# Performance work log

Measured on AMD Instinct MI355X. Metric: run time of the kernel, lower is better.

## Reference

```python
import jax, jax.numpy as jnp
import numpy as np

R = 8
EPS = 1e-08
EPSS = 1e-12


def _diff_x(x, r):
    left = x[:, :, r:2 * r + 1]
    middle = x[:, :, 2 * r + 1:] - x[:, :, :-2 * r - 1]
    right = x[:, :, -1:] - x[:, :, -2 * r - 1:-r - 1]
    return jnp.concatenate([left, middle, right], axis=2)


def _diff_y(x, r):
    left = x[:, :, :, r:2 * r + 1]
    middle = x[:, :, :, 2 * r + 1:] - x[:, :, :, :-2 * r - 1]
    right = x[:, :, :, -1:] - x[:, :, :, -2 * r - 1:-r - 1]
    return jnp.concatenate([left, middle, right], axis=3)


def box_filter(x, r):
    # cumsum-based (2r+1)x(2r+1) box sum with clamped borders (matches torch BoxFilter)
    return _diff_y(jnp.cumsum(_diff_x(jnp.cumsum(x, axis=2), r), axis=3), r)


def bilinear_resize(x, H, W):
    # F.interpolate(mode='bilinear', align_corners=True) for NCHW
    n, c, h, w = x.shape
    ys = jnp.linspace(0.0, h - 1.0, H)
    xs = jnp.linspace(0.0, w - 1.0, W)
    y0 = jnp.floor(ys).astype(jnp.int32)
    x0 = jnp.floor(xs).astype(jnp.int32)
    y1 = jnp.minimum(y0 + 1, h - 1)
    x1 = jnp.minimum(x0 + 1, w - 1)
    wy = (ys - y0).astype(x.dtype)[None, None, :, None]
    wx = (xs - x0).astype(x.dtype)[None, None, None, :]
    rows = jnp.take(x, y0, axis=2) * (1.0 - wy) + jnp.take(x, y1, axis=2) * wy
    return jnp.take(rows, x0, axis=3) * (1.0 - wx) + jnp.take(rows, x1, axis=3) * wx


def setup_inputs() -> dict:
    key = jax.random.key(0)
    k1, k2, k3, k4 = jax.random.split(key, 4)
    return {
        "lr_x": jax.random.normal(k1, (4, 3, 256, 256), dtype=jnp.float32),
        "lr_y": jax.random.normal(k2, (4, 3, 256, 256), dtype=jnp.float32),
        "hr_x": jax.random.normal(k3, (4, 3, 1024, 1024), dtype=jnp.float32),
        "l_a": jax.random.uniform(k4, (4, 3, 256, 256), dtype=jnp.float32),
    }


def reference(lr_x, lr_y, hr_x, l_a):
    n, c, h, w = lr_x.shape
    _, _, hh, wh = hr_x.shape
    dt = lr_x.dtype

    N = box_filter(jnp.ones((1, 1, h, w), dtype=dt), R)  # local window counts

    l_a = jnp.abs(l_a) + EPSS
    l_t = l_a / jnp.sum(l_a)

    mean_a = box_filter(l_a) if False else box_filter(l_a, R) / N
    mean_a2xy = box_filter(l_a * l_a * lr_x * lr_y, R) / N
    mean_tax = box_filter(l_t * l_a * lr_x, R) / N
    mean_ay = box_filter(l_a * lr_y, R) / N
    mean_a2x2 = box_filter(l_a * l_a * lr_x * lr_x, R) / N
    mean_ax = box_filter(l_a * lr_x, R) / N

    temp = jnp.abs(mean_a2x2 - N * mean_tax * mean_ax)
    A = (mean_a2xy - N * mean_tax * mean_ay) / (temp + EPS)
    b = (mean_ay - A * mean_ax) / mean_a

    A = box_filter(A, R) / N
    b = box_filter(b, R) / N

    mean_A = bilinear_resize(A, hh, wh)
    mean_b = bilinear_resize(b, hh, wh)
    return (mean_A * hr_x + mean_b).astype(jnp.float32)
```

## Files before the change

kernel.cpp:

```cpp
#include <hip/hip_runtime.h>

#define RAD 8
#define HH 256
#define WW 256
#define NC 12
#define PS (HH*WW)

__global__ __launch_bounds__(256) void k_hbox6(const float* __restrict__ la,
                                               const float* __restrict__ lx,
                                               const float* __restrict__ ly,
                                               float* __restrict__ Hbuf,
                                               float* __restrict__ sumS) {
    int p  = blockIdx.x >> 6;
    int rc = blockIdx.x & 63;
    int base = p * PS + rc * 4 * WW;
    int tid = threadIdx.x, lane = tid & 63, wid = tid >> 6;
    __shared__ float wtot[6][4];
    __shared__ float Pref[6][WW];
    __shared__ float ls[4];
    float asum = 0.0f;
    int  j1    = min(tid + RAD, WW - 1);
    bool hasj0 = (tid - RAD) > 0;
    int  j0m1  = tid - RAD - 1;
    for (int rr = 0; rr < 4; rr++) {
        int o = base + rr * WW + tid;
        float a  = fabsf(la[o]) + 1e-12f;
        float xv = lx[o];
        float yv = ly[o];
        asum += a;
        float ax = a * xv, ay = a * yv;
        float v0 = a, v1 = ax, v2 = ay, v3 = a * ax, v4 = ax * ax, v5 = ax * ay;
        #pragma unroll
        for (int off = 1; off < 64; off <<= 1) {
            float t0 = __shfl_up(v0, off, 64), t1 = __shfl_up(v1, off, 64),
                  t2 = __shfl_up(v2, off, 64), t3 = __shfl_up(v3, off, 64),
                  t4 = __shfl_up(v4, off, 64), t5 = __shfl_up(v5, off, 64);
            if (lane >= off) { v0 += t0; v1 += t1; v2 += t2; v3 += t3; v4 += t4; v5 += t5; }
        }
        if (lane == 63) {
            wtot[0][wid] = v0; wtot[1][wid] = v1; wtot[2][wid] = v2;
            wtot[3][wid] = v3; wtot[4][wid] = v4; wtot[5][wid] = v5;
        }
        __syncthreads();
        float a0 = 0, a1 = 0, a2 = 0, a3 = 0, a4 = 0, a5 = 0;
        for (int w = 0; w < wid; w++) {
            a0 += wtot[0][w]; a1 += wtot[1][w]; a2 += wtot[2][w];
            a3 += wtot[3][w]; a4 += wtot[4][w]; a5 += wtot[5][w];
        }
        Pref[0][tid] = v0 + a0; Pref[1][tid] = v1 + a1; Pref[2][tid] = v2 + a2;
        Pref[3][tid] = v3 + a3; Pref[4][tid] = v4 + a4; Pref[5][tid] = v5 + a5;
        __syncthreads();
        #pragma unroll
        for (int k = 0; k < 6; k++) {
            float s = Pref[k][j1] - (hasj0 ? Pref[k][j0m1] : 0.0f);
            Hbuf[k * NC * PS + o] = s;
        }
    }
    for (int off = 32; off > 0; off >>= 1) asum += __shfl_down(asum, off, 64);
    if (lane == 0) ls[wid] = asum;
    __syncthreads();
    if (tid == 0) atomicAdd(sumS, ls[0] + ls[1] + ls[2] + ls[3]);
}

__global__ __launch_bounds__(256) void k_vab(const float* __restrict__ Hbuf,
                                             const float* __restrict__ sumS,
                                             float* __restrict__ HA,
                                             float* __restrict__ HB) {
    int p  = blockIdx.x >> 5;
    int i0 = (blockIdx.x & 31) * 8;
    int tid = threadIdx.x, lane = tid & 63, wid = tid >> 6;
    __shared__ float wtot[2][4];
    __shared__ float Pref[2][WW];
    float invS = 1.0f / sumS[0];
    const float* Hp = Hbuf + p * PS + tid;
    float s0 = 0, s1 = 0, s2 = 0, s3 = 0, s4 = 0, s5 = 0;
    int lo = max(i0 - RAD, 0), hi = min(i0 + RAD, HH - 1);
    for (int i = lo; i <= hi; i++) {
        int o = i * WW;
        s0 += Hp[0 * NC * PS + o]; s1 += Hp[1 * NC * PS + o]; s2 += Hp[2 * NC * PS + o];
        s3 += Hp[3 * NC * PS + o]; s4 += Hp[4 * NC * PS + o]; s5 += Hp[5 * NC * PS + o];
    }
    float cx = (float)(min(tid + RAD, WW - 1) - max(tid - RAD, 0) + 1);
    int  j1    = min(tid + RAD, WW - 1);
    bool hasj0 = (tid - RAD) > 0;
    int  j0m1  = tid - RAD - 1;
    for (int i = i0; i < i0 + 8; i++) {
        if (i > i0) {
            int add = i + RAD, sub = i - RAD - 1;
            if (add <= HH - 1) {
                int o = add * WW;
                s0 += Hp[0 * NC * PS + o]; s1 += Hp[1 * NC * PS + o]; s2 += Hp[2 * NC * PS + o];
                s3 += Hp[3 * NC * PS + o]; s4 += Hp[4 * NC * PS + o]; s5 += Hp[5 * NC * PS + o];
            }
            if (sub >= 0) {
                int o = sub * WW;
                s0 -= Hp[0 * NC * PS + o]; s1 -= Hp[1 * NC * PS + o]; s2 -= Hp[2 * NC * PS + o];
                s3 -= Hp[3 * NC * PS + o]; s4 -= Hp[4 * NC * PS + o]; s5 -= Hp[5 * NC * PS + o];
            }
        }
        float cy = (float)(min(i + RAD, HH - 1) - max(i - RAD, 0) + 1);
        float Nv = cx * cy;
        float invN = 1.0f / Nv;
        float mean_a    = s0 * invN;
        float mean_ax   = s1 * invN;
        float mean_ay   = s2 * invN;
        float mean_tax  = s3 * invN * invS;
        float mean_a2x2 = s4 * invN;
        float mean_a2xy = s5 * invN;
        float temp = fabsf(mean_a2x2 - Nv * mean_tax * mean_ax);
        float Av = (mean_a2xy - Nv * mean_tax * mean_ay) / (temp + 1e-8f);
        float bv = (mean_ay - Av * mean_ax) / mean_a;
        float v0 = Av, v1 = bv;
        #pragma unroll
        for (int off = 1; off < 64; off <<= 1) {
            float t0 = __shfl_up(v0, off, 64), t1 = __shfl_up(v1, off, 64);
            if (lane >= off) { v0 += t0; v1 += t1; }
        }
        if (lane == 63) { wtot[0][wid] = v0; wtot[1][wid] = v1; }
        __syncthreads();
        float a0 = 0, a1 = 0;
        for (int w = 0; w < wid; w++) { a0 += wtot[0][w]; a1 += wtot[1][w]; }
        Pref[0][tid] = v0 + a0; Pref[1][tid] = v1 + a1;
        __syncthreads();
        int o = p * PS + i * WW + tid;
        HA[o] = Pref[0][j1] - (hasj0 ? Pref[0][j0m1] : 0.0f);
        HB[o] = Pref[1][j1] - (hasj0 ? Pref[1][j0m1] : 0.0f);
    }
}

__global__ __launch_bounds__(256) void k_vbox2(const float* __restrict__ HA,
                                               const float* __restrict__ HB,
                                               float* __restrict__ mA,
                                               float* __restrict__ mB) {
    int p  = blockIdx.x >> 5;
    int i0 = (blockIdx.x & 31) * 8;
    int col = threadIdx.x;
    const float* a = HA + p * PS + col;
    const float* b = HB + p * PS + col;
    float sa = 0, sb = 0;
    int lo = max(i0 - RAD, 0), hi = min(i0 + RAD, HH - 1);
    for (int i = lo; i <= hi; i++) { sa += a[i * WW]; sb += b[i * WW]; }
    float cx = (float)(min(col + RAD, WW - 1) - max(col - RAD, 0) + 1);
    for (int i = i0; i < i0 + 8; i++) {
        if (i > i0) {
            if (i + RAD <= HH - 1) { sa += a[(i + RAD) * WW]; sb += b[(i + RAD) * WW]; }
            if (i - RAD - 1 >= 0)  { sa -= a[(i - RAD - 1) * WW]; sb -= b[(i - RAD - 1) * WW]; }
        }
        float cy = (float)(min(i + RAD, HH - 1) - max(i - RAD, 0) + 1);
        float inv = 1.0f / (cx * cy);
        mA[p * PS + i * WW + col] = sa * inv;
        mB[p * PS + i * WW + col] = sb * inv;
    }
}

__global__ __launch_bounds__(256) void k_resize(const float* __restrict__ mA,
                                                const float* __restrict__ mB,
                                                const float* __restrict__ hrx,
                                                float* __restrict__ out) {
    int idx = blockIdx.x * 256 + threadIdx.x;
    int p   = idx >> 18;
    int rem = idx & ((1 << 18) - 1);
    int I   = rem >> 8;
    int J4  = (rem & 255) << 2;
    const float scale = 255.0f / 1023.0f;
    float ysf = (float)I * scale;
    int   y0  = (int)ysf;
    float wy  = ysf - (float)y0;
    int   y1  = min(y0 + 1, HH - 1);
    const float* a0p = mA + p * PS + y0 * WW;
    const float* a1p = mA + p * PS + y1 * WW;
    const float* b0p = mB + p * PS + y0 * WW;
    const float* b1p = mB + p * PS + y1 * WW;
    int xb = (int)((float)J4 * scale);
    int i1 = min(xb + 1, WW - 1);
    int i2 = min(xb + 2, WW - 1);
    float A0a = a0p[xb], A0b = a0p[i1], A0c = a0p[i2];
    float A1a = a1p[xb], A1b = a1p[i1], A1c = a1p[i2];
    float B0a = b0p[xb], B0b = b0p[i1], B0c = b0p[i2];
    float B1a = b1p[xb], B1b = b1p[i1], B1c = b1p[i2];
    float4 h = ((const float4*)hrx)[idx];
    float hv[4] = {h.x, h.y, h.z, h.w};
    float ov[4];
    float omwy = 1.0f - wy;
    #pragma unroll
    for (int k = 0; k < 4; k++) {
        float xsk = (float)(J4 + k) * scale;
        int   x0  = (int)xsk;
        float wx  = xsk - (float)x0;
        bool hisel = (x0 > xb);
        float Alo0 = hisel ? A0b : A0a, Ahi0 = hisel ? A0c : A0b;
        float Alo1 = hisel ? A1b : A1a, Ahi1 = hisel ? A1c : A1b;
        float Blo0 = hisel ? B0b : B0a, Bhi0 = hisel ? B0c : B0b;
        float Blo1 = hisel ? B1b : B1a, Bhi1 = hisel ? B1c : B1b;
        float omwx = 1.0f - wx;
        float Ar0 = Alo0 * omwx + Ahi0 * wx;
        float Ar1 = Alo1 * omwx + Ahi1 * wx;
        float Br0 = Blo0 * omwx + Bhi0 * wx;
        float Br1 = Blo1 * omwx + Bhi1 * wx;
        float Avv = Ar0 * omwy + Ar1 * wy;
        float Bvv = Br0 * omwy + Br1 * wy;
        ov[k] = Avv * hv[k] + Bvv;
    }
    float4 o;
    o.x = ov[0]; o.y = ov[1]; o.z = ov[2]; o.w = ov[3];
    ((float4*)out)[idx] = o;
}

extern "C" void kernel_launch(void* const* d_in, const int* in_sizes, int n_in,
                              void* d_out, int out_size, void* d_ws, size_t ws_size,
                              hipStream_t stream) {
    const float* lr_x = (const float*)d_in[0];
    const float* lr_y = (const float*)d_in[1];
    const float* hr_x = (const float*)d_in[2];
    const float* l_a  = (const float*)d_in[3];
    float* out = (float*)d_out;

    float* ws   = (float*)d_ws;
    float* sumS = ws;
    float* Hbuf = ws + 64;
    float* HA   = Hbuf + 6 * NC * PS;
    float* HB   = HA + NC * PS;
    float* mA   = HB + NC * PS;
    float* mB   = mA + NC * PS;

    hipMemsetAsync(sumS, 0, 256, stream);

    k_hbox6 <<<NC * 64, 256, 0, stream>>>(l_a, lr_x, lr_y, Hbuf, sumS);
    k_vab   <<<NC * 32, 256, 0, stream>>>(Hbuf, sumS, HA, HB);
    k_vbox2 <<<NC * 32, 256, 0, stream>>>(HA, HB, mA, mB);
    k_resize<<<(NC * 1024 * 1024 / 4) / 256, 256, 0, stream>>>(mA, mB, hr_x, out);
}
```

Measured before the change: 168.1 us.

## Fuse second box filter into A/b kernel and replace atomic sum with partials

Merges the A/b computation and the second vertical box filter into one kernel. Each block recomputes A/b rows for a halo of 8 rows on either side of its tile and keeps them in a 17-row shared-memory ring buffer for the sliding vertical sum. This removes the HA/HB global round trip, one kernel launch and the memset. The global sum of l_a now comes from per-block partial sums reduced inside the consumer kernel, replacing the atomicAdd. The cost is roughly three times as many A/b rows computed per block (24 instead of 8), each with its own scan and barriers, plus extra shared memory.

```diff
diff --git a/kernel.cpp b/kernel.cpp
--- a/kernel.cpp
+++ b/kernel.cpp
@@ -10,7 +10,7 @@
                                                const float* __restrict__ lx,
                                                const float* __restrict__ ly,
                                                float* __restrict__ Hbuf,
-                                               float* __restrict__ sumS) {
+                                               float* __restrict__ partials) {
     int p  = blockIdx.x >> 6;
     int rc = blockIdx.x & 63;
     int base = p * PS + rc * 4 * WW;
@@ -59,34 +59,56 @@
     for (int off = 32; off > 0; off >>= 1) asum += __shfl_down(asum, off, 64);
     if (lane == 0) ls[wid] = asum;
     __syncthreads();
-    if (tid == 0) atomicAdd(sumS, ls[0] + ls[1] + ls[2] + ls[3]);
-}
-
-__global__ __launch_bounds__(256) void k_vab(const float* __restrict__ Hbuf,
-                                             const float* __restrict__ sumS,
-                                             float* __restrict__ HA,
-                                             float* __restrict__ HB) {
+    if (tid == 0) partials[blockIdx.x] = ls[0] + ls[1] + ls[2] + ls[3];
+}
+
+__global__ __launch_bounds__(256) void k_vab2(const float* __restrict__ Hbuf,
+                                              const float* __restrict__ partials,
+                                              float* __restrict__ mA,
+                                              float* __restrict__ mB) {
     int p  = blockIdx.x >> 5;
     int i0 = (blockIdx.x & 31) * 8;
     int tid = threadIdx.x, lane = tid & 63, wid = tid >> 6;
     __shared__ float wtot[2][4];
     __shared__ float Pref[2][WW];
-    float invS = 1.0f / sumS[0];
+    __shared__ float ringA[17][WW];
+    __shared__ float ringB[17][WW];
+    __shared__ float ls[4];
+    __shared__ float sS;
+
+    float psum = partials[tid] + partials[tid + 256] + partials[tid + 512];
+    for (int off = 32; off > 0; off >>= 1) psum += __shfl_down(psum, off, 64);
+    if (lane == 0) ls[wid] = psum;
+    __syncthreads();
+    if (tid == 0) sS = ls[0] + ls[1] + ls[2] + ls[3];
+    __syncthreads();
+    float invS = 1.0f / sS;
+
     const float* Hp = Hbuf + p * PS + tid;
+    int jA0 = max(i0 - RAD, 0);
+    int jA1 = min(i0 + 8 + RAD - 1, HH - 1);
+
     float s0 = 0, s1 = 0, s2 = 0, s3 = 0, s4 = 0, s5 = 0;
-    int lo = max(i0 - RAD, 0), hi = min(i0 + RAD, HH - 1);
-    for (int i = lo; i <= hi; i++) {
-        int o = i * WW;
-        s0 += Hp[0 * NC * PS + o]; s1 += Hp[1 * NC * PS + o]; s2 += Hp[2 * NC * PS + o];
-        s3 += Hp[3 * NC * PS + o]; s4 += Hp[4 * NC * PS + o]; s5 += Hp[5 * NC * PS + o];
+    {
+        int lo = max(jA0 - RAD, 0), hi = min(jA0 + RAD, HH - 1);
+        for (int i = lo; i <= hi; i++) {
+            int o = i * WW;
+            s0 += Hp[0 * NC * PS + o]; s1 += Hp[1 * NC * PS + o]; s2 += Hp[2 * NC * PS + o];
+            s3 += Hp[3 * NC * PS + o]; s4 += Hp[4 * NC * PS + o]; s5 += Hp[5 * NC * PS + o];
+        }
     }
     float cx = (float)(min(tid + RAD, WW - 1) - max(tid - RAD, 0) + 1);
-    int  j1    = min(tid + RAD, WW - 1);
+    int  j1c   = min(tid + RAD, WW - 1);
     bool hasj0 = (tid - RAD) > 0;
     int  j0m1  = tid - RAD - 1;
-    for (int i = i0; i < i0 + 8; i++) {
-        if (i > i0) {
-            int add = i + RAD, sub = i - RAD - 1;
+
+    float sa = 0.0f, sb = 0.0f;
+    int cnt = 0;
+    int r = i0, rend = i0 + 8;
+
+    for (int j = jA0; j <= jA1; j++) {
+        if (j > jA0) {
+            int add = j + RAD, sub = j - RAD - 1;
             if (add <= HH - 1) {
                 int o = add * WW;
                 s0 += Hp[0 * NC * PS + o]; s1 += Hp[1 * NC * PS + o]; s2 += Hp[2 * NC * PS + o];
@@ -98,7 +120,7 @@
                 s3 -= Hp[3 * NC * PS + o]; s4 -= Hp[4 * NC * PS + o]; s5 -= Hp[5 * NC * PS + o];
             }
         }
-        float cy = (float)(min(i + RAD, HH - 1) - max(i - RAD, 0) + 1);
+        float cy = (float)(min(j + RAD, HH - 1) - max(j - RAD, 0) + 1);
         float Nv = cx * cy;
         float invN = 1.0f / Nv;
         float mean_a    = s0 * invN;
@@ -110,6 +132,7 @@
         float temp = fabsf(mean_a2x2 - Nv * mean_tax * mean_ax);
         float Av = (mean_a2xy - Nv * mean_tax * mean_ay) / (temp + 1e-8f);
         float bv = (mean_ay - Av * mean_ax) / mean_a;
+
         float v0 = Av, v1 = bv;
         #pragma unroll
         for (int off = 1; off < 64; off <<= 1) {
@@ -122,34 +145,33 @@
         for (int w = 0; w < wid; w++) { a0 += wtot[0][w]; a1 += wtot[1][w]; }
         Pref[0][tid] = v0 + a0; Pref[1][tid] = v1 + a1;
         __syncthreads();
-        int o = p * PS + i * WW + tid;
-        HA[o] = Pref[0][j1] - (hasj0 ? Pref[0][j0m1] : 0.0f);
-        HB[o] = Pref[1][j1] - (hasj0 ? Pref[1][j0m1] : 0.0f);
-    }
-}
-
-__global__ __launch_bounds__(256) void k_vbox2(const float* __restrict__ HA,
-                                               const float* __restrict__ HB,
-                                               float* __restrict__ mA,
-                                               float* __restrict__ mB) {
-    int p  = blockIdx.x >> 5;
-    int i0 = (blockIdx.x & 31) * 8;
-    int col = threadIdx.x;
-    const float* a = HA + p * PS + col;
-    const float* b = HB + p * PS + col;
-    float sa = 0, sb = 0;
-    int lo = max(i0 - RAD, 0), hi = min(i0 + RAD, HH - 1);
-    for (int i = lo; i <= hi; i++) { sa += a[i * WW]; sb += b[i * WW]; }
-    float cx = (float)(min(col + RAD, WW - 1) - max(col - RAD, 0) + 1);
-    for (int i = i0; i < i0 + 8; i++) {
-        if (i > i0) {
-            if (i + RAD <= HH - 1) { sa += a[(i + RAD) * WW]; sb += b[(i + RAD) * WW]; }
-            if (i - RAD - 1 >= 0)  { sa -= a[(i - RAD - 1) * WW]; sb -= b[(i - RAD - 1) * WW]; }
-        }
-        float cy = (float)(min(i + RAD, HH - 1) - max(i - RAD, 0) + 1);
-        float inv = 1.0f / (cx * cy);
-        mA[p * PS + i * WW + col] = sa * inv;
-        mB[p * PS + i * WW + col] = sb * inv;
+        float HAj = Pref[0][j1c] - (hasj0 ? Pref[0][j0m1] : 0.0f);
+        float HBj = Pref[1][j1c] - (hasj0 ? Pref[1][j0m1] : 0.0f);
+
+        int slot = cnt % 17;
+        if (cnt >= 17) { sa -= ringA[slot][tid]; sb -= ringB[slot][tid]; }
+        ringA[slot][tid] = HAj; ringB[slot][tid] = HBj;
+        sa += HAj; sb += HBj;
+        cnt++;
+
+        while (r < rend && (j == r + RAD || j == HH - 1)) {
+            float cy2 = (float)(min(r + RAD, HH - 1) - max(r - RAD, 0) + 1);
+            float inv = 1.0f / (cx * cy2);
+            int o = p * PS + r * WW + tid;
+            mA[o] = sa * inv;
+            mB[o] = sb * inv;
+            r++;
+            if (r < rend && j == HH - 1) {
+                int rowout = r - 1 - RAD;
+                if (rowout >= jA0) {
+                    int so = (rowout - jA0) % 17;
+                    sa -= ringA[so][tid];
+                    sb -= ringB[so][tid];
+                }
+            } else {
+                break;
+            }
+        }
     }
 }
 
@@ -215,18 +237,13 @@
     const float* l_a  = (const float*)d_in[3];
     float* out = (float*)d_out;
 
-    float* ws   = (float*)d_ws;
-    float* sumS = ws;
-    float* Hbuf = ws + 64;
-    float* HA   = Hbuf + 6 * NC * PS;
-    float* HB   = HA + NC * PS;
-    float* mA   = HB + NC * PS;
-    float* mB   = mA + NC * PS;
-
-    hipMemsetAsync(sumS, 0, 256, stream);
-
-    k_hbox6 <<<NC * 64, 256, 0, stream>>>(l_a, lr_x, lr_y, Hbuf, sumS);
-    k_vab   <<<NC * 32, 256, 0, stream>>>(Hbuf, sumS, HA, HB);
-    k_vbox2 <<<NC * 32, 256, 0, stream>>>(HA, HB, mA, mB);
+    float* ws       = (float*)d_ws;
+    float* partials = ws;
+    float* Hbuf     = ws + 1024;
+    float* mA       = Hbuf + 6 * NC * PS;
+    float* mB       = mA + NC * PS;
+
+    k_hbox6 <<<NC * 64, 256, 0, stream>>>(l_a, lr_x, lr_y, Hbuf, partials);
+    k_vab2  <<<NC * 32, 256, 0, stream>>>(Hbuf, partials, mA, mB);
     k_resize<<<(NC * 1024 * 1024 / 4) / 256, 256, 0, stream>>>(mA, mB, hr_x, out);
 }
```

New measurement: 175.3 us. +4.3%, slower.
